# Optimization experiments

Measured on AMD Instinct MI355X. Metric: run time of the kernel, lower is better.

Reference implementation:

```python
import jax, jax.numpy as jnp
import numpy as np

N = 4096            # number of graph nodes (keypoints)
L_MAX = 6
Q = 2
D, H, W = 64, 128, 128
ST = 0.15           # sigma_transition
SP = 0.3            # sigma_pairwise
AU = 1.0            # alpha_unary
L = len(range(0, 2 * L_MAX + 1, Q)) ** 3   # 343 displacement labels


def setup_inputs() -> dict:
    key = jax.random.key(0)
    k1, k2 = jax.random.split(key)
    unary = jax.random.normal(k1, (N, L), dtype=jnp.float32)
    u = jax.random.uniform(k2, (N, N), dtype=jnp.float32)
    dist = (u + u.T) * 0.5  # symmetric pairwise distance matrix
    # Buffer A exactly as in __init__: displacement grid -> RBF transition kernel
    r = np.arange(0, 2 * L_MAX + 1, Q, dtype=np.float32)
    g = np.stack(np.meshgrid(r, r, r, indexing='ij'), axis=3).reshape(-1, 3) - L_MAX
    disp = g[:, ::-1] * 2.0 / np.array([W - 1, H - 1, D - 1], dtype=np.float32)
    A = np.exp(-((disp[:, None, :] - disp[None, :, :]) ** 2).sum(-1) / (2.0 * ST ** 2))
    return {"unary": unary, "dist": dist, "A": jnp.asarray(A, dtype=jnp.float32)}


def _forward(unary, dist, A):
    n, l = unary.shape
    unary = AU * unary
    pairwise = jnp.exp(-dist / (2.0 * SP ** 2))
    INF = jnp.float32(1e30)
    idx = jnp.arange(n)
    d = dist.at[idx, idx].set(INF)  # no self edges

    # ---- Prim's MST rooted at node 0 (addition order = parents-before-children) ----
    in_tree0 = jnp.zeros((n,), dtype=bool).at[0].set(True)
    best0 = d[0]                      # cheapest edge from each node into the tree
    parent0 = jnp.zeros((n,), jnp.int32)
    order0 = jnp.zeros((n,), jnp.int32)

    def prim_body(i, st):
        in_tree, best, parent, order = st
        nxt = jnp.argmin(jnp.where(in_tree, INF, best)).astype(jnp.int32)
        in_tree = in_tree.at[nxt].set(True)
        order = order.at[i].set(nxt)
        upd = (d[nxt] < best) & ~in_tree
        parent = jnp.where(upd, nxt, parent)
        best = jnp.where(upd, d[nxt], best)
        return (in_tree, best, parent, order)

    _, _, parent, order = jax.lax.fori_loop(1, n, prim_body, (in_tree0, best0, parent0, order0))
    root = order[0]  # == 0

    # ---- Upward (leaves -> root) max-sum Viterbi messages along tree edges ----
    ptr0 = jnp.zeros((n, l), jnp.int32)

    def up(carry, c):
        belief, ptr = carry
        p = parent[c]
        # scores[l_c, l_p] = belief[c, l_c] + pairwise(c,p) * A[l_c, l_p]
        scores = belief[c][:, None] + pairwise[c, p] * A
        msg = scores.max(axis=0)                                   # [L]
        ptr = ptr.at[c].set(jnp.argmax(scores, axis=0).astype(jnp.int32))
        belief = belief.at[p].add(jnp.where(c == root, 0.0, msg))  # root sends nothing
        return (belief, ptr), None

    (belief, ptr), _ = jax.lax.scan(up, (unary, ptr0), order[::-1])

    # ---- Downward backtracking (root -> leaves) ----
    def down(labels, c):
        lab = jnp.where(c == root,
                        jnp.argmax(belief[root]).astype(jnp.int32),
                        ptr[c, labels[parent[c]]])
        return labels.at[c].set(lab), None

    labels, _ = jax.lax.scan(down, jnp.zeros((n,), jnp.int32), order)

    # disp_out = -1 everywhere, +1 at selected label, scaled by 1e5
    onehot = jax.nn.one_hot(labels, l, dtype=unary.dtype)
    return (2.0 * onehot - 1.0) * 100000.0


def reference(unary, dist, A):
    return _forward(unary, dist, A)
```

## Files before the change

kernel.cpp:

```cpp
#include <hip/hip_runtime.h>
#include <hip/hip_cooperative_groups.h>
#include <math.h>

namespace cg = cooperative_groups;
typedef unsigned long long u64;

#define NN 4096
#define LBL 343
#define PSTRIDE 344
#define APITCH 344
#define U64MAX 0xFFFFFFFFFFFFFFFFull
#define MST_ROUNDS 12

__global__ void mrf_init_kernel(const float* __restrict__ A, float* __restrict__ Apad,
                                int* __restrict__ compA,
                                u64* __restrict__ minEa, u64* __restrict__ minEb,
                                int* __restrict__ counters)
{
  const int id = blockIdx.x * 256 + threadIdx.x;
  if (id < NN) { compA[id] = id; minEa[id] = U64MAX; minEb[id] = U64MAX; }
  if (id == 0) { counters[0] = NN; counters[1] = NN; counters[2] = 0; }
  if (id < LBL * APITCH) {
    const int r = id / APITCH;
    const int c = id - r * APITCH;
    Apad[id] = (c < LBL) ? A[r * LBL + c] : 0.0f;
  }
}

__global__ __launch_bounds__(1024) void mrf_scan_kernel(
    const float* __restrict__ dist, const int* __restrict__ compR,
    u64* __restrict__ minE, int* __restrict__ counters, int round)
{
  __shared__ int s_cc[16];
  __shared__ u64 s_cv[16];

  if (blockIdx.x == 0 && threadIdx.x == 0) counters[round & 1] = 0;
  if (round > 0 && counters[(round - 1) & 1] <= 1) return;

  const int i    = (blockIdx.x * 1024 + threadIdx.x) >> 6;
  const int lane = threadIdx.x & 63;
  const int wib  = threadIdx.x >> 6;

  const int ci = compR[i];
  const float4* rowp = (const float4*)(dist + (size_t)i * NN);
  const int4* cp = (const int4*)compR;
  u64 best = U64MAX;
  #pragma unroll 4
  for (int k = 0; k < 16; ++k) {
    const int q = k * 64 + lane;
    const float4 dv = rowp[q];
    const int4 cv = cp[q];
    const int j0 = q * 4;
    if (cv.x != ci) { const u64 p = ((u64)__float_as_uint(dv.x) << 24) | ((u64)i << 12) | (u64)(j0    ); best = best < p ? best : p; }
    if (cv.y != ci) { const u64 p = ((u64)__float_as_uint(dv.y) << 24) | ((u64)i << 12) | (u64)(j0 + 1); best = best < p ? best : p; }
    if (cv.z != ci) { const u64 p = ((u64)__float_as_uint(dv.z) << 24) | ((u64)i << 12) | (u64)(j0 + 2); best = best < p ? best : p; }
    if (cv.w != ci) { const u64 p = ((u64)__float_as_uint(dv.w) << 24) | ((u64)i << 12) | (u64)(j0 + 3); best = best < p ? best : p; }
  }
  #pragma unroll
  for (int sh = 32; sh >= 1; sh >>= 1) {
    const u64 o = __shfl_down(best, sh);
    best = best < o ? best : o;
  }
  if (lane == 0) {
    s_cc[wib] = (best == U64MAX) ? -1 : ci;
    s_cv[wib] = best;
  }
  __syncthreads();
  if (threadIdx.x == 0) {
    for (int a = 0; a < 16; ++a) {
      const int c = s_cc[a];
      if (c < 0) continue;
      bool dup = false;
      for (int b2 = 0; b2 < a; ++b2) if (s_cc[b2] == c) { dup = true; break; }
      if (dup) continue;
      u64 b = s_cv[a];
      for (int b2 = a + 1; b2 < 16; ++b2)
        if (s_cc[b2] == c && s_cv[b2] < b) b = s_cv[b2];
      atomicMin(&minE[c & (NN - 1)], b);
    }
  }
}

__global__ __launch_bounds__(1024) void mrf_hook_kernel(
    const int* __restrict__ compR, int* __restrict__ compW,
    const u64* __restrict__ minE, u64* __restrict__ minEnext,
    int* __restrict__ eu, int* __restrict__ ev, unsigned* __restrict__ ew,
    int* __restrict__ counters, int round)
{
  if (round > 0 && counters[(round - 1) & 1] <= 1) return;
  const int i = blockIdx.x * 1024 + threadIdx.x;
  if (i >= NN) return;
  minEnext[i] = U64MAX;

  const int r0 = compR[i];
  int cur = r0;
  for (int guard = 0; guard < NN + 2; ++guard) {
    const u64 e = minE[cur];
    if (e == U64MAX) break;
    const int v = (int)(e & 0xFFF);
    const int t = compR[v];
    if (t == cur) break;
    const u64 te = minE[t];
    if (te != U64MAX) {
      const int tv = (int)(te & 0xFFF);
      if (compR[tv] == cur && cur < t) break;
    }
    cur = t;
  }
  compW[i] = cur;
  if (cur == i) atomicAdd(&counters[round & 1], 1);

  if (r0 == i) {
    const u64 e = minE[i];
    if (e != U64MAX) {
      const int v = (int)(e & 0xFFF);
      const int u = (int)((e >> 12) & 0xFFF);
      const unsigned wb = (unsigned)(e >> 24);
      const int t = compR[v];
      bool mutual = false;
      const u64 te = minE[t];
      if (te != U64MAX) {
        const int tv = (int)(te & 0xFFF);
        mutual = (compR[tv] == i);
      }
      if (!(mutual && i < t)) {
        const int slot = atomicAdd(&counters[2], 1);
        if (slot < NN) { eu[slot] = u; ev[slot] = v; ew[slot] = wb; }
      }
    }
  }
}

__device__ __forceinline__ void scan4096(int* arr, int* tmp16, int tid)
{
  __syncthreads();
  const int base = tid * 4;
  const int c0 = arr[base], c1 = arr[base + 1], c2 = arr[base + 2], c3 = arr[base + 3];
  const int lsum = c0 + c1 + c2 + c3;
  const int lane = tid & 63, wid = tid >> 6;
  int incl = lsum;
  #pragma unroll
  for (int o = 1; o < 64; o <<= 1) {
    const int t = __shfl_up(incl, o);
    if (lane >= o) incl += t;
  }
  if (lane == 63) tmp16[wid] = incl;
  __syncthreads();
  if (tid == 0) {
    int run = 0;
    for (int w = 0; w < 16; ++w) { const int t = tmp16[w]; tmp16[w] = run; run += t; }
  }
  __syncthreads();
  const int excl = tmp16[wid] + incl - lsum;
  arr[base]     = excl;
  arr[base + 1] = excl + c0;
  arr[base + 2] = excl + c0 + c1;
  arr[base + 3] = excl + c0 + c1 + c2;
  __syncthreads();
}

__global__ __launch_bounds__(1024) void mrf_root_kernel(
    const float* __restrict__ dist,
    const int* __restrict__ eu, const int* __restrict__ ev, const unsigned* __restrict__ ew,
    int* __restrict__ parent_g, int* __restrict__ childStart, int* __restrict__ childList,
    int* __restrict__ levStart, int* __restrict__ levNodes, int* __restrict__ segList,
    int* __restrict__ meta, float* __restrict__ w_edge,
    int* __restrict__ ready, int* __restrict__ cursor)
{
  __shared__ int s_deg[NN];
  __shared__ int s_start[NN];
  __shared__ int s_cur[NN];
  __shared__ int s_parent[NN];
  __shared__ unsigned short s_dep[NN];
  __shared__ unsigned short s_fr[2][NN];
  __shared__ u64 s_adj[2 * (NN - 1)];
  __shared__ int s_tmp16[16];
  __shared__ int s_fcnt, s_nf;

  const int tid = threadIdx.x;

  for (int j = tid; j < NN; j += 1024) ready[j] = 0;
  if (tid == 0) cursor[0] = 0;

  for (int j = tid; j < NN; j += 1024) s_deg[j] = 0;
  __syncthreads();
  for (int e = tid; e < NN - 1; e += 1024) {
    atomicAdd(&s_deg[eu[e] & (NN - 1)], 1);
    atomicAdd(&s_deg[ev[e] & (NN - 1)], 1);
  }
  __syncthreads();
  for (int j = tid; j < NN; j += 1024) s_start[j] = s_deg[j];
  scan4096(s_start, s_tmp16, tid);
  for (int j = tid; j < NN; j += 1024) s_cur[j] = s_start[j];
  __syncthreads();
  for (int e = tid; e < NN - 1; e += 1024) {
    const int u = eu[e] & (NN - 1), v = ev[e] & (NN - 1);
    const u64 wb = (u64)ew[e];
    const int p1 = atomicAdd(&s_cur[u], 1);
    s_adj[p1 & (2 * NN - 1)] = (wb << 12) | (u64)v;
    const int p2 = atomicAdd(&s_cur[v], 1);
    s_adj[p2 & (2 * NN - 1)] = (wb << 12) | (u64)u;
  }
  for (int j = tid; j < NN; j += 1024) { s_parent[j] = 0; s_dep[j] = 0; }
  if (tid == 0) { s_fcnt = 1; s_nf = 0; s_fr[0][0] = 0; }
  __syncthreads();

  if (tid < 64) {
    int cur = 0, lev = 0;
    while (true) {
      asm volatile("s_waitcnt lgkmcnt(0)" ::: "memory");
      __builtin_amdgcn_sched_barrier(0);
      const int fcnt = s_fcnt;
      if (fcnt == 0) break;
      for (int idx = tid; idx < fcnt; idx += 64) {
        const int x = s_fr[cur][idx];
        const int st = s_start[x], dg = s_deg[x];
        for (int a = 0; a < dg; ++a) {
          const u64 ent = s_adj[(st + a) & (2 * NN - 1)];
          const int nb = (int)(ent & 0xFFF);
          if (nb != s_parent[x] || x == 0) {
            s_parent[nb] = x;
            s_dep[nb] = (unsigned short)(lev + 1);
            const int slot = atomicAdd(&s_nf, 1);
            s_fr[1 - cur][slot] = (unsigned short)nb;
          }
        }
      }
      asm volatile("s_waitcnt lgkmcnt(0)" ::: "memory");
      __builtin_amdgcn_sched_barrier(0);
      if (tid == 0) { s_fcnt = s_nf; s_nf = 0; }
      ++lev;
      cur ^= 1;
    }
    if (tid == 0) s_fcnt = lev;
  }
  __syncthreads();
  const int numLev = s_fcnt;
  if (tid == 0) { s_parent[0] = 0; meta[0] = numLev; }
  __syncthreads();

  int* s_cs2 = (int*)s_fr;
  for (int j = tid; j < NN; j += 1024) s_cs2[j] = s_deg[j] - (j != 0 ? 1 : 0);
  scan4096(s_cs2, s_tmp16, tid);
  for (int j = tid; j < NN; j += 1024) childStart[j] = s_cs2[j];
  if (tid == 0) childStart[NN] = NN - 1;
  __syncthreads();

  for (int p = tid; p < NN; p += 1024) {
    const int st = s_start[p], dg = s_deg[p], cs = s_cs2[p];
    const int par = s_parent[p];
    u64 buf[16];
    int m = 0;
    for (int a = 0; a < dg; ++a) {
      const u64 ent = s_adj[(st + a) & (2 * NN - 1)];
      const int nb = (int)(ent & 0xFFF);
      if (p != 0 && nb == par) continue;
      if (m < 16) {
        int q = m;
        while (q > 0 && buf[q - 1] < ent) { buf[q] = buf[q - 1]; --q; }
        buf[q] = ent;
        ++m;
      } else {
        childList[cs + m] = nb;
        ++m;
      }
    }
    const int lim = m < 16 ? m : 16;
    for (int k = 0; k < lim; ++k) childList[cs + k] = (int)(buf[k] & 0xFFF);
  }

  for (int j = tid; j < NN; j += 1024) s_cur[j] = 0;
  __syncthreads();
  for (int j = tid; j < NN; j += 1024) atomicAdd(&s_cur[s_dep[j]], 1);
  scan4096(s_cur, s_tmp16, tid);
  for (int j = tid; j < NN; j += 1024) { levStart[j] = s_cur[j]; s_start[j] = s_cur[j]; }
  if (tid == 0) levStart[NN] = NN;
  __syncthreads();
  for (int j = tid; j < NN; j += 1024) {
    const int pos = atomicAdd(&s_start[s_dep[j]], 1);
    levNodes[pos] = j;
  }
  __syncthreads();

  if (tid == 0) s_nf = 0;
  for (int j = tid; j < NN; j += 1024) s_cur[j] = 0;
  __syncthreads();
  for (int j = tid; j < NN; j += 1024) {
    const int ce = (j == NN - 1) ? (NN - 1) : s_cs2[j + 1];
    int key = -1;
    if (ce - s_cs2[j] == 0) {
      int c = j;
      while (c != 0) {
        const int par = s_parent[c];
        if (childList[s_cs2[par]] != c) break;
        c = par;
      }
      key = s_dep[c];
      atomicAdd(&s_cur[numLev - 1 - key], 1);
      atomicAdd(&s_nf, 1);
    }
    s_deg[j] = key;
  }
  scan4096(s_cur, s_tmp16, tid);
  for (int j = tid; j < NN; j += 1024) s_start[j] = s_cur[j];
  __syncthreads();
  for (int j = tid; j < NN; j += 1024) {
    const int key = s_deg[j];
    if (key >= 0) {
      const int pos = atomicAdd(&s_start[numLev - 1 - key], 1);
      segList[pos] = j;
    }
  }
  if (tid == 0) meta[1] = s_nf;

  for (int j = tid; j < NN; j += 1024) {
    parent_g[j] = s_parent[j];
    w_edge[j] = (j == 0) ? 0.0f
                         : expf(-dist[(size_t)j * NN + s_parent[j]] / 0.18f);
  }
}

__global__ __launch_bounds__(768) void mrf_solve_kernel(
    const float* __restrict__ unary, const float* __restrict__ Apad,
    float* __restrict__ msgbuf, unsigned short* __restrict__ ptrbuf,
    const int* __restrict__ parent, const int* __restrict__ childStart,
    const int* __restrict__ childList, const int* __restrict__ levStart,
    const int* __restrict__ levNodes, const int* __restrict__ segList,
    const float* __restrict__ w_edge,
    int* __restrict__ labels, const int* __restrict__ meta,
    int* __restrict__ ready, int* __restrict__ cursor)
{
  __shared__ float s_b[APITCH];
  __shared__ float s_pv[8][APITCH];
  __shared__ int   s_pi[8][APITCH];
  __shared__ int   s_lab[NN];
  __shared__ int   s_sidx;
  const int tid = threadIdx.x;
  const bool act = (tid < 688);
  const int t = act ? (tid % 86) : 0;
  const int h = act ? (tid / 86) : 0;
  const int lc0 = h * 43;
  const int lc1 = (h == 7) ? LBL : (lc0 + 43);

  int numLev = meta[0];
  if (numLev < 1) numLev = 1;
  if (numLev > NN) numLev = NN;
  int numSegs = meta[1];
  if (numSegs < 1) numSegs = 1;
  if (numSegs > NN) numSegs = NN;

  bool didRoot = false;

  while (!didRoot) {
    if (tid == 0) s_sidx = atomicAdd(cursor, 1);
    __syncthreads();
    const int sidx = s_sidx;
    if (sidx >= numSegs) break;

    int v = segList[sidx] & (NN - 1);
    if (tid < LBL) s_b[tid] = unary[(size_t)v * LBL + tid];
    __syncthreads();

    while (true) {
      if (v == 0) {
        if (tid == 0) {
          float bv = s_b[0]; int bi = 0;
          for (int l = 1; l < LBL; ++l)
            if (s_b[l] > bv) { bv = s_b[l]; bi = l; }
          labels[0] = bi;
          s_lab[0] = bi;
        }
        __syncthreads();
        didRoot = true;
        break;
      }

      if (act) {
        const float w = w_edge[v];
        const float4* __restrict__ Ap4 = (const float4*)Apad;
        float4 a = Ap4[(size_t)lc0 * 86 + t];
        float sb = s_b[lc0];
        float bv0 = __fadd_rn(sb, __fmul_rn(w, a.x));
        float bv1 = __fadd_rn(sb, __fmul_rn(w, a.y));
        float bv2 = __fadd_rn(sb, __fmul_rn(w, a.z));
        float bv3 = __fadd_rn(sb, __fmul_rn(w, a.w));
        int bi0 = lc0, bi1 = lc0, bi2 = lc0, bi3 = lc0;
        #pragma unroll 2
        for (int lc = lc0 + 1; lc < lc1; ++lc) {
          const float4 av = Ap4[(size_t)lc * 86 + t];
          const float sbl = s_b[lc];
          const float s0 = __fadd_rn(sbl, __fmul_rn(w, av.x));
          const float s1 = __fadd_rn(sbl, __fmul_rn(w, av.y));
          const float s2 = __fadd_rn(sbl, __fmul_rn(w, av.z));
          const float s3 = __fadd_rn(sbl, __fmul_rn(w, av.w));
          if (s0 > bv0) { bv0 = s0; bi0 = lc; }
          if (s1 > bv1) { bv1 = s1; bi1 = lc; }
          if (s2 > bv2) { bv2 = s2; bi2 = lc; }
          if (s3 > bv3) { bv3 = s3; bi3 = lc; }
        }
        const int lpb = t * 4;
        s_pv[h][lpb + 0] = bv0; s_pi[h][lpb + 0] = bi0;
        s_pv[h][lpb + 1] = bv1; s_pi[h][lpb + 1] = bi1;
        s_pv[h][lpb + 2] = bv2; s_pi[h][lpb + 2] = bi2;
        s_pv[h][lpb + 3] = bv3; s_pi[h][lpb + 3] = bi3;
      }
      __syncthreads();

      float fbv = 0.0f;
      if (tid < LBL) {
        fbv = s_pv[0][tid];
        int fbi = s_pi[0][tid];
        #pragma unroll
        for (int hh = 1; hh < 8; ++hh) {
          const float pv = s_pv[hh][tid];
          if (pv > fbv) { fbv = pv; fbi = s_pi[hh][tid]; }
        }
        s_pi[0][tid] = fbi;
      }
      __syncthreads();

      if (tid < 172) {
        const unsigned lo = (unsigned)s_pi[0][2 * tid] & 0xFFFFu;
        const unsigned hi = (2 * tid + 1 < LBL)
                              ? ((unsigned)s_pi[0][2 * tid + 1] & 0xFFFFu) : 0u;
        __hip_atomic_store((unsigned*)(ptrbuf + (size_t)v * PSTRIDE + 2 * tid),
                           lo | (hi << 16),
                           __ATOMIC_RELAXED, __HIP_MEMORY_SCOPE_AGENT);
      }

      const int p = parent[v] & (NN - 1);
      const int csp = childStart[p];
      int degp = childStart[p + 1] - csp;
      if (degp < 1) degp = 1;
      if (degp > 64) degp = 64;
      const bool isCarrier = ((childList[csp] & (NN - 1)) == v);

      if (!isCarrier) {
        if (tid < LBL)
          __hip_atomic_store((unsigned*)&msgbuf[(size_t)v * LBL + tid],
                             __float_as_uint(fbv),
                             __ATOMIC_RELAXED, __HIP_MEMORY_SCOPE_AGENT);
        __syncthreads();
        if (tid == 0)
          __hip_atomic_fetch_add(&ready[p], 1,
                                 __ATOMIC_RELEASE, __HIP_MEMORY_SCOPE_AGENT);
        break;
      }

      if (degp > 1 && tid == 0) {
        long long guard = 0;
        while (__hip_atomic_load(&ready[p], __ATOMIC_RELAXED,
                                 __HIP_MEMORY_SCOPE_AGENT) < degp - 1) {
          __builtin_amdgcn_s_sleep(1);
          if (++guard > 30000000LL) break;
        }
      }
      __syncthreads();

      if (tid < LBL) {
        float nb = __fadd_rn(unary[(size_t)p * LBL + tid], fbv);
        for (int k = 1; k < degp; ++k) {
          const int ch = childList[csp + k] & (NN - 1);
          const unsigned um = __hip_atomic_load(
              (const unsigned*)&msgbuf[(size_t)ch * LBL + tid],
              __ATOMIC_RELAXED, __HIP_MEMORY_SCOPE_AGENT);
          nb = __fadd_rn(nb, __uint_as_float(um));
        }
        s_b[tid] = nb;
      }
      v = p;
      __syncthreads();
    }
  }

  if (!didRoot) return;
  __syncthreads();
  for (int lev = 1; lev < numLev; ++lev) {
    int ls = levStart[lev], le = levStart[lev + 1];
    if (ls < 0) ls = 0;
    if (le > NN) le = NN;
    for (int idx = ls + tid; idx < le; idx += 768) {
      const int c = levNodes[idx] & (NN - 1);
      int pl = s_lab[parent[c] & (NN - 1)];
      if (pl < 0) pl = 0;
      if (pl >= LBL) pl = LBL - 1;
      const unsigned pk = __hip_atomic_load(
          (const unsigned*)(ptrbuf + (size_t)c * PSTRIDE + (pl & ~1)),
          __ATOMIC_RELAXED, __HIP_MEMORY_SCOPE_AGENT);
      const int lab = (pl & 1) ? (int)(pk >> 16) : (int)(pk & 0xFFFFu);
      s_lab[c] = lab;
      labels[c] = lab;
    }
    __syncthreads();
  }
}

__global__ void mrf_out_kernel(const int* __restrict__ labels, float* __restrict__ out)
{
  const int id = blockIdx.x * blockDim.x + threadIdx.x;
  if (id >= NN * LBL) return;
  const int c = id / LBL;
  const int l = id - c * LBL;
  out[id] = (l == labels[c]) ? 100000.0f : -100000.0f;
}

extern "C" void kernel_launch(void* const* d_in, const int* in_sizes, int n_in,
                              void* d_out, int out_size, void* d_ws, size_t ws_size,
                              hipStream_t stream)
{
  (void)in_sizes; (void)n_in; (void)out_size; (void)ws_size;
  const float* unary = (const float*)d_in[0];
  const float* dist  = (const float*)d_in[1];
  const float* A     = (const float*)d_in[2];
  float* out = (float*)d_out;

  char* ws = (char*)d_ws;
  size_t off = 0;
  auto take = [&](size_t bytes) -> void* {
    void* p = (void*)(ws + off);
    off += (bytes + 255) & ~(size_t)255;
    return p;
  };
  float* msgbuf = out;
  unsigned short* ptrbuf = (unsigned short*)take((size_t)NN * PSTRIDE * sizeof(unsigned short));
  float*    Apad       = (float*)   take((size_t)LBL * APITCH * sizeof(float));
  int*      compA      = (int*)     take(NN * sizeof(int));
  int*      compB      = (int*)     take(NN * sizeof(int));
  u64*      minEa      = (u64*)     take(NN * sizeof(u64));
  u64*      minEb      = (u64*)     take(NN * sizeof(u64));
  int*      eu         = (int*)     take(NN * sizeof(int));
  int*      ev         = (int*)     take(NN * sizeof(int));
  unsigned* ew         = (unsigned*)take(NN * sizeof(unsigned));
  int*      counters   = (int*)     take(256);
  int*      parent     = (int*)     take(NN * sizeof(int));
  int*      childStart = (int*)     take((NN + 1) * sizeof(int));
  int*      childList  = (int*)     take(NN * sizeof(int));
  int*      levStart   = (int*)     take((NN + 1) * sizeof(int));
  int*      levNodes   = (int*)     take(NN * sizeof(int));
  int*      segList    = (int*)     take(NN * sizeof(int));
  int*      labels     = (int*)     take(NN * sizeof(int));
  int*      meta       = (int*)     take(256);
  float*    w_edge     = (float*)   take(NN * sizeof(float));
  int*      ready      = (int*)     take(NN * sizeof(int));
  int*      cursor     = (int*)     take(256);

  hipLaunchKernelGGL(mrf_init_kernel, dim3((LBL * APITCH + 255) / 256), dim3(256),
                     0, stream, A, Apad, compA, minEa, minEb, counters);

  for (int r = 0; r < MST_ROUNDS; ++r) {
    const int* compR = (r & 1) ? compB : compA;
    int*       compW = (r & 1) ? compA : compB;
    u64*       mcur  = (r & 1) ? minEb : minEa;
    u64*       mnext = (r & 1) ? minEa : minEb;
    hipLaunchKernelGGL(mrf_scan_kernel, dim3(256), dim3(1024), 0, stream,
                       dist, compR, mcur, counters, r);
    hipLaunchKernelGGL(mrf_hook_kernel, dim3(4), dim3(1024), 0, stream,
                       compR, compW, mcur, mnext, eu, ev, ew, counters, r);
  }

  hipLaunchKernelGGL(mrf_root_kernel, dim3(1), dim3(1024), 0, stream,
                     dist, eu, ev, ew, parent, childStart, childList,
                     levStart, levNodes, segList, meta, w_edge,
                     ready, cursor);

  {
    void* args[] = {
      (void*)&unary, (void*)&Apad, (void*)&msgbuf, (void*)&ptrbuf,
      (void*)&parent, (void*)&childStart, (void*)&childList,
      (void*)&levStart, (void*)&levNodes, (void*)&segList, (void*)&w_edge,
      (void*)&labels, (void*)&meta, (void*)&ready, (void*)&cursor
    };
    hipLaunchCooperativeKernel((void*)mrf_solve_kernel, dim3(256), dim3(768),
                               args, 0, stream);
  }

  const int total = NN * LBL;
  hipLaunchKernelGGL(mrf_out_kernel, dim3((total + 255) / 256), dim3(256), 0, stream,
                     labels, out);
}
```

Before: 907.0 us.

## Recompute backtrack argmax from stored beliefs instead of storing argmax pointers

The upward pass now keeps only max values (fmaxf) and stores each node's full belief vector, dropping the per-label argmax tracking and the packed pointer table. A new chain-parallel downward kernel walks segments from the top, waits on the parent's label, and recomputes argmax over one row of A per node using warp shuffles. The level-ordered backtrack and its level lists are removed. This lightens the critical upward loop, at the cost of a separate launch, spin-waiting across chains, and extra belief storage.

```diff
diff --git a/kernel.cpp b/kernel.cpp
--- a/kernel.cpp
+++ b/kernel.cpp
@@ -7,7 +7,6 @@
 
 #define NN 4096
 #define LBL 343
-#define PSTRIDE 344
 #define APITCH 344
 #define U64MAX 0xFFFFFFFFFFFFFFFFull
 #define MST_ROUNDS 12
@@ -163,9 +162,9 @@
     const float* __restrict__ dist,
     const int* __restrict__ eu, const int* __restrict__ ev, const unsigned* __restrict__ ew,
     int* __restrict__ parent_g, int* __restrict__ childStart, int* __restrict__ childList,
-    int* __restrict__ levStart, int* __restrict__ levNodes, int* __restrict__ segList,
+    int* __restrict__ segList, int* __restrict__ segTop,
     int* __restrict__ meta, float* __restrict__ w_edge,
-    int* __restrict__ ready, int* __restrict__ cursor)
+    int* __restrict__ ready, int* __restrict__ cursor, int* __restrict__ labels)
 {
   __shared__ int s_deg[NN];
   __shared__ int s_start[NN];
@@ -179,8 +178,8 @@
 
   const int tid = threadIdx.x;
 
-  for (int j = tid; j < NN; j += 1024) ready[j] = 0;
-  if (tid == 0) cursor[0] = 0;
+  for (int j = tid; j < NN; j += 1024) { ready[j] = 0; labels[j] = -1; }
+  if (tid == 0) { cursor[0] = 0; cursor[16] = 0; }
 
   for (int j = tid; j < NN; j += 1024) s_deg[j] = 0;
   __syncthreads();
@@ -268,18 +267,6 @@
     const int lim = m < 16 ? m : 16;
     for (int k = 0; k < lim; ++k) childList[cs + k] = (int)(buf[k] & 0xFFF);
   }
-
-  for (int j = tid; j < NN; j += 1024) s_cur[j] = 0;
-  __syncthreads();
-  for (int j = tid; j < NN; j += 1024) atomicAdd(&s_cur[s_dep[j]], 1);
-  scan4096(s_cur, s_tmp16, tid);
-  for (int j = tid; j < NN; j += 1024) { levStart[j] = s_cur[j]; s_start[j] = s_cur[j]; }
-  if (tid == 0) levStart[NN] = NN;
-  __syncthreads();
-  for (int j = tid; j < NN; j += 1024) {
-    const int pos = atomicAdd(&s_start[s_dep[j]], 1);
-    levNodes[pos] = j;
-  }
   __syncthreads();
 
   if (tid == 0) s_nf = 0;
@@ -307,8 +294,15 @@
   for (int j = tid; j < NN; j += 1024) {
     const int key = s_deg[j];
     if (key >= 0) {
+      int c = j;
+      while (c != 0) {
+        const int par = s_parent[c];
+        if (childList[s_cs2[par]] != c) break;
+        c = par;
+      }
       const int pos = atomicAdd(&s_start[numLev - 1 - key], 1);
       segList[pos] = j;
+      segTop[pos]  = c;
     }
   }
   if (tid == 0) meta[1] = s_nf;
@@ -322,18 +316,15 @@
 
 __global__ __launch_bounds__(768) void mrf_solve_kernel(
     const float* __restrict__ unary, const float* __restrict__ Apad,
-    float* __restrict__ msgbuf, unsigned short* __restrict__ ptrbuf,
+    float* __restrict__ msgbuf, float* __restrict__ belief,
     const int* __restrict__ parent, const int* __restrict__ childStart,
-    const int* __restrict__ childList, const int* __restrict__ levStart,
-    const int* __restrict__ levNodes, const int* __restrict__ segList,
+    const int* __restrict__ childList, const int* __restrict__ segList,
     const float* __restrict__ w_edge,
     int* __restrict__ labels, const int* __restrict__ meta,
     int* __restrict__ ready, int* __restrict__ cursor)
 {
   __shared__ float s_b[APITCH];
   __shared__ float s_pv[8][APITCH];
-  __shared__ int   s_pi[8][APITCH];
-  __shared__ int   s_lab[NN];
   __shared__ int   s_sidx;
   const int tid = threadIdx.x;
   const bool act = (tid < 688);
@@ -342,9 +333,6 @@
   const int lc0 = h * 43;
   const int lc1 = (h == 7) ? LBL : (lc0 + 43);
 
-  int numLev = meta[0];
-  if (numLev < 1) numLev = 1;
-  if (numLev > NN) numLev = NN;
   int numSegs = meta[1];
   if (numSegs < 1) numSegs = 1;
   if (numSegs > NN) numSegs = NN;
@@ -362,13 +350,14 @@
     __syncthreads();
 
     while (true) {
+      if (tid < LBL) belief[(size_t)v * LBL + tid] = s_b[tid];
+
       if (v == 0) {
         if (tid == 0) {
           float bv = s_b[0]; int bi = 0;
           for (int l = 1; l < LBL; ++l)
             if (s_b[l] > bv) { bv = s_b[l]; bi = l; }
           labels[0] = bi;
-          s_lab[0] = bi;
         }
         __syncthreads();
         didRoot = true;
@@ -384,48 +373,28 @@
         float bv1 = __fadd_rn(sb, __fmul_rn(w, a.y));
         float bv2 = __fadd_rn(sb, __fmul_rn(w, a.z));
         float bv3 = __fadd_rn(sb, __fmul_rn(w, a.w));
-        int bi0 = lc0, bi1 = lc0, bi2 = lc0, bi3 = lc0;
         #pragma unroll 2
         for (int lc = lc0 + 1; lc < lc1; ++lc) {
           const float4 av = Ap4[(size_t)lc * 86 + t];
           const float sbl = s_b[lc];
-          const float s0 = __fadd_rn(sbl, __fmul_rn(w, av.x));
-          const float s1 = __fadd_rn(sbl, __fmul_rn(w, av.y));
-          const float s2 = __fadd_rn(sbl, __fmul_rn(w, av.z));
-          const float s3 = __fadd_rn(sbl, __fmul_rn(w, av.w));
-          if (s0 > bv0) { bv0 = s0; bi0 = lc; }
-          if (s1 > bv1) { bv1 = s1; bi1 = lc; }
-          if (s2 > bv2) { bv2 = s2; bi2 = lc; }
-          if (s3 > bv3) { bv3 = s3; bi3 = lc; }
+          bv0 = fmaxf(bv0, __fadd_rn(sbl, __fmul_rn(w, av.x)));
+          bv1 = fmaxf(bv1, __fadd_rn(sbl, __fmul_rn(w, av.y)));
+          bv2 = fmaxf(bv2, __fadd_rn(sbl, __fmul_rn(w, av.z)));
+          bv3 = fmaxf(bv3, __fadd_rn(sbl, __fmul_rn(w, av.w)));
         }
         const int lpb = t * 4;
-        s_pv[h][lpb + 0] = bv0; s_pi[h][lpb + 0] = bi0;
-        s_pv[h][lpb + 1] = bv1; s_pi[h][lpb + 1] = bi1;
-        s_pv[h][lpb + 2] = bv2; s_pi[h][lpb + 2] = bi2;
-        s_pv[h][lpb + 3] = bv3; s_pi[h][lpb + 3] = bi3;
+        s_pv[h][lpb + 0] = bv0;
+        s_pv[h][lpb + 1] = bv1;
+        s_pv[h][lpb + 2] = bv2;
+        s_pv[h][lpb + 3] = bv3;
       }
       __syncthreads();
 
       float fbv = 0.0f;
       if (tid < LBL) {
         fbv = s_pv[0][tid];
-        int fbi = s_pi[0][tid];
         #pragma unroll
-        for (int hh = 1; hh < 8; ++hh) {
-          const float pv = s_pv[hh][tid];
-          if (pv > fbv) { fbv = pv; fbi = s_pi[hh][tid]; }
-        }
-        s_pi[0][tid] = fbi;
-      }
-      __syncthreads();
-
-      if (tid < 172) {
-        const unsigned lo = (unsigned)s_pi[0][2 * tid] & 0xFFFFu;
-        const unsigned hi = (2 * tid + 1 < LBL)
-                              ? ((unsigned)s_pi[0][2 * tid + 1] & 0xFFFFu) : 0u;
-        __hip_atomic_store((unsigned*)(ptrbuf + (size_t)v * PSTRIDE + 2 * tid),
-                           lo | (hi << 16),
-                           __ATOMIC_RELAXED, __HIP_MEMORY_SCOPE_AGENT);
+        for (int hh = 1; hh < 8; ++hh) fbv = fmaxf(fbv, s_pv[hh][tid]);
       }
 
       const int p = parent[v] & (NN - 1);
@@ -472,26 +441,90 @@
       __syncthreads();
     }
   }
-
-  if (!didRoot) return;
-  __syncthreads();
-  for (int lev = 1; lev < numLev; ++lev) {
-    int ls = levStart[lev], le = levStart[lev + 1];
-    if (ls < 0) ls = 0;
-    if (le > NN) le = NN;
-    for (int idx = ls + tid; idx < le; idx += 768) {
-      const int c = levNodes[idx] & (NN - 1);
-      int pl = s_lab[parent[c] & (NN - 1)];
-      if (pl < 0) pl = 0;
+}
+
+__global__ __launch_bounds__(64) void mrf_down_kernel(
+    const float* __restrict__ belief, const float* __restrict__ Apad,
+    const int* __restrict__ parent, const int* __restrict__ childStart,
+    const int* __restrict__ childList, const float* __restrict__ w_edge,
+    const int* __restrict__ segTop, int* __restrict__ labels,
+    const int* __restrict__ meta, int* __restrict__ cursor)
+{
+  const int lane = threadIdx.x;
+  int numSegs = meta[1];
+  if (numSegs < 1) numSegs = 1;
+  if (numSegs > NN) numSegs = NN;
+
+  while (true) {
+    int my = 0;
+    if (lane == 0) my = atomicAdd(&cursor[16], 1);
+    my = __shfl(my, 0);
+    if (my >= numSegs) break;
+    const int sidx = numSegs - 1 - my;
+
+    int v = segTop[sidx] & (NN - 1);
+    int pl = 0;
+    if (v == 0) {
+      pl = labels[0];
+      const int cs = childStart[0];
+      if (childStart[1] - cs <= 0) continue;
+      v = childList[cs] & (NN - 1);
+    } else {
+      const int par = parent[v] & (NN - 1);
+      if (lane == 0) {
+        long long guard = 0;
+        do {
+          pl = __hip_atomic_load(&labels[par], __ATOMIC_RELAXED,
+                                 __HIP_MEMORY_SCOPE_AGENT);
+          if (pl >= 0) break;
+          __builtin_amdgcn_s_sleep(1);
+        } while (++guard < 30000000LL);
+      }
+      pl = __shfl(pl, 0);
+    }
+    if (pl < 0) pl = 0;
+
+    float b[6];
+    {
+      int nb = 0;
+      for (int lc = lane; lc < LBL; lc += 64) b[nb++] = belief[(size_t)v * LBL + lc];
+    }
+
+    while (true) {
       if (pl >= LBL) pl = LBL - 1;
-      const unsigned pk = __hip_atomic_load(
-          (const unsigned*)(ptrbuf + (size_t)c * PSTRIDE + (pl & ~1)),
-          __ATOMIC_RELAXED, __HIP_MEMORY_SCOPE_AGENT);
-      const int lab = (pl & 1) ? (int)(pk >> 16) : (int)(pk & 0xFFFFu);
-      s_lab[c] = lab;
-      labels[c] = lab;
-    }
-    __syncthreads();
+      const int cs = childStart[v];
+      const int deg = childStart[v + 1] - cs;
+      const int nxt = (deg > 0) ? (childList[cs] & (NN - 1)) : -1;
+      float pb[6];
+      if (nxt >= 0) {
+        int nb = 0;
+        for (int lc = lane; lc < LBL; lc += 64) pb[nb++] = belief[(size_t)nxt * LBL + lc];
+      }
+
+      const float w = w_edge[v];
+      const float* __restrict__ Ar = Apad + (size_t)pl * APITCH;
+      float bv = -3.4e38f; int bi = 0x3FFFFF;
+      int nb = 0;
+      for (int lc = lane; lc < LBL; lc += 64) {
+        const float s = __fadd_rn(b[nb++], __fmul_rn(w, Ar[lc]));
+        if (s > bv) { bv = s; bi = lc; }
+      }
+      #pragma unroll
+      for (int sh = 32; sh >= 1; sh >>= 1) {
+        const float ov = __shfl_down(bv, sh);
+        const int   oi = __shfl_down(bi, sh);
+        if (ov > bv || (ov == bv && oi < bi)) { bv = ov; bi = oi; }
+      }
+      bi = __shfl(bi, 0);
+      if (lane == 0)
+        __hip_atomic_store(&labels[v], bi,
+                           __ATOMIC_RELAXED, __HIP_MEMORY_SCOPE_AGENT);
+      if (nxt < 0) break;
+      pl = bi;
+      v = nxt;
+      #pragma unroll
+      for (int q = 0; q < 6; ++q) b[q] = pb[q];
+    }
   }
 }
 
@@ -501,7 +534,8 @@
   if (id >= NN * LBL) return;
   const int c = id / LBL;
   const int l = id - c * LBL;
-  out[id] = (l == labels[c]) ? 100000.0f : -100000.0f;
+  const int lab = labels[c];
+  out[id] = (l == lab) ? 100000.0f : -100000.0f;
 }
 
 extern "C" void kernel_launch(void* const* d_in, const int* in_sizes, int n_in,
@@ -522,7 +556,7 @@
     return p;
   };
   float* msgbuf = out;
-  unsigned short* ptrbuf = (unsigned short*)take((size_t)NN * PSTRIDE * sizeof(unsigned short));
+  float*    belief     = (float*)   take((size_t)NN * LBL * sizeof(float));
   float*    Apad       = (float*)   take((size_t)LBL * APITCH * sizeof(float));
   int*      compA      = (int*)     take(NN * sizeof(int));
   int*      compB      = (int*)     take(NN * sizeof(int));
@@ -535,9 +569,8 @@
   int*      parent     = (int*)     take(NN * sizeof(int));
   int*      childStart = (int*)     take((NN + 1) * sizeof(int));
   int*      childList  = (int*)     take(NN * sizeof(int));
-  int*      levStart   = (int*)     take((NN + 1) * sizeof(int));
-  int*      levNodes   = (int*)     take(NN * sizeof(int));
   int*      segList    = (int*)     take(NN * sizeof(int));
+  int*      segTop     = (int*)     take(NN * sizeof(int));
   int*      labels     = (int*)     take(NN * sizeof(int));
   int*      meta       = (int*)     take(256);
   float*    w_edge     = (float*)   take(NN * sizeof(float));
@@ -560,20 +593,29 @@
 
   hipLaunchKernelGGL(mrf_root_kernel, dim3(1), dim3(1024), 0, stream,
                      dist, eu, ev, ew, parent, childStart, childList,
-                     levStart, levNodes, segList, meta, w_edge,
-                     ready, cursor);
+                     segList, segTop, meta, w_edge, ready, cursor, labels);
 
   {
     void* args[] = {
-      (void*)&unary, (void*)&Apad, (void*)&msgbuf, (void*)&ptrbuf,
+      (void*)&unary, (void*)&Apad, (void*)&msgbuf, (void*)&belief,
       (void*)&parent, (void*)&childStart, (void*)&childList,
-      (void*)&levStart, (void*)&levNodes, (void*)&segList, (void*)&w_edge,
+      (void*)&segList, (void*)&w_edge,
       (void*)&labels, (void*)&meta, (void*)&ready, (void*)&cursor
     };
     hipLaunchCooperativeKernel((void*)mrf_solve_kernel, dim3(256), dim3(768),
                                args, 0, stream);
   }
 
+  {
+    void* args[] = {
+      (void*)&belief, (void*)&Apad, (void*)&parent, (void*)&childStart,
+      (void*)&childList, (void*)&w_edge, (void*)&segTop,
+      (void*)&labels, (void*)&meta, (void*)&cursor
+    };
+    hipLaunchCooperativeKernel((void*)mrf_down_kernel, dim3(256), dim3(64),
+                               args, 0, stream);
+  }
+
   const int total = NN * LBL;
   hipLaunchKernelGGL(mrf_out_kernel, dim3((total + 255) / 256), dim3(256), 0, stream,
                      labels, out);
```

New measurement: 1.048 ms. 15.6% more time.
